# Kernel optimization log

Hardware: AMD Instinct MI355X
Metric: run time of the kernel (lower is better)

## Reference

```python
import jax, jax.numpy as jnp
import numpy as np

TOP_K = 8
THRESHOLD = 0.0        # similarity_threshold
SELF_SIM = 0.999       # exclude_self cutoff
EPS = 1e-12            # F.normalize eps


def _l2_normalize(x):
    # matches torch.nn.functional.normalize(p=2, dim=-1, eps=1e-12)
    n = jnp.linalg.norm(x, axis=-1, keepdims=True)
    return x / jnp.maximum(n, EPS)


def setup_inputs() -> dict:
    key = jax.random.key(0)
    kq, km = jax.random.split(key)
    B, N, D = 2048, 65536, 512
    q = jax.random.normal(kq, (B, D), dtype=jnp.float32)
    mem = jax.random.normal(km, (N, D), dtype=jnp.float32)
    # add_memories() stores L2-normalized representations when normalize=True
    mem = _l2_normalize(mem)
    return {"query_representations": q, "memory_bank": mem}


def reference(query_representations, memory_bank):
    # normalize queries (config.normalize_memories=True)
    q = _l2_normalize(query_representations)            # [B, D]
    # cosine similarity: bank rows already unit-norm
    sims = jnp.einsum("bd,nd->bn", q, memory_bank)      # [B, N]
    neg_inf = jnp.float32(-jnp.inf)
    # exclude_self: mask near-exact matches
    sims = jnp.where(sims > SELF_SIM, neg_inf, sims)
    # threshold mask
    sims = jnp.where(sims >= THRESHOLD, sims, neg_inf)
    # top-k (k = min(top_k, count) = TOP_K since bank is full)
    top_sims, top_idx = jax.lax.top_k(sims, TOP_K)      # [B, K]
    retrieved = memory_bank[top_idx]                    # [B, K, D] gather
    mask = top_sims > neg_inf                           # [B, K] valid entries
    return retrieved, top_sims, mask
```

## Files before the change

### kernel.cpp

```cpp
#include <hip/hip_runtime.h>
#include <math.h>

#define D        512
#define NQ       2048
#define NMEM     65536
#define TOPK     8
#define NCAND    32
#define SELF_SIM 0.999f
#define FSCALE   64.0f
#define TAU_RAW  483.328f
#define CAP      448
#define SCAP     1280

#define QB     256
#define SPAN   1024
#define NSPL   64
#define NROUND 64
#define BUFSZ  24576u

typedef __attribute__((ext_vector_type(4))) float f32x4;

__device__ __forceinline__ void gl_lds16(const void* g, void* l) {
    __builtin_amdgcn_global_load_lds(
        (const __attribute__((address_space(1))) void*)g,
        (__attribute__((address_space(3))) void*)l, 16, 0, 0);
}

__device__ __forceinline__ unsigned pack4_fp8(float4 v) {
    int lo = __builtin_amdgcn_cvt_pk_fp8_f32(v.x * FSCALE, v.y * FSCALE, 0, false);
    return (unsigned)__builtin_amdgcn_cvt_pk_fp8_f32(v.z * FSCALE, v.w * FSCALE, lo, true);
}

__global__ __launch_bounds__(256)
void k_prep(const float* __restrict__ mem, const float* __restrict__ q,
            unsigned* __restrict__ mp8, unsigned* __restrict__ qp8,
            double* __restrict__ qinv)
{
    if (blockIdx.x < 2048) {
        const int n16 = (NMEM * D) / 16;
        for (int i = blockIdx.x * 256 + threadIdx.x; i < n16; i += 2048 * 256) {
            const float4* p = (const float4*)(mem + (size_t)i * 16);
            uint4 o;
            o.x = pack4_fp8(p[0]); o.y = pack4_fp8(p[1]);
            o.z = pack4_fp8(p[2]); o.w = pack4_fp8(p[3]);
            ((uint4*)mp8)[i] = o;
        }
    } else {
        const int row  = (blockIdx.x - 2048) * 4 + (threadIdx.x >> 6);
        const int lane = threadIdx.x & 63;
        const float4* src = (const float4*)(q + (size_t)row * D);
        float4 v0 = src[lane];
        float4 v1 = src[lane + 64];
        double ss = (double)v0.x*v0.x + (double)v0.y*v0.y + (double)v0.z*v0.z + (double)v0.w*v0.w
                  + (double)v1.x*v1.x + (double)v1.y*v1.y + (double)v1.z*v1.z + (double)v1.w*v1.w;
        #pragma unroll
        for (int off = 32; off >= 1; off >>= 1)
            ss += __shfl_xor(ss, off, 64);
        double inv = 1.0 / fmax(sqrt(ss), 1e-12);
        float invf = (float)inv;
        float4 n0 = make_float4(v0.x*invf, v0.y*invf, v0.z*invf, v0.w*invf);
        float4 n1 = make_float4(v1.x*invf, v1.y*invf, v1.z*invf, v1.w*invf);
        unsigned* dst = qp8 + (size_t)row * (D / 4);
        dst[lane]      = pack4_fp8(n0);
        dst[lane + 64] = pack4_fp8(n1);
        if (lane == 0) qinv[row] = inv;
    }
}

__global__ __launch_bounds__(512, 4)
void k_cand(const char* __restrict__ qp8, const char* __restrict__ mp8,
            unsigned* __restrict__ cnt, uint2* __restrict__ cbuf)
{
    __shared__ __align__(16) char smem[49152 + 16 + SCAP * 8];
    unsigned* scnt = (unsigned*)(smem + 49152);
    uint2*    sbuf = (uint2*)   (smem + 49168);

    const int tid = threadIdx.x;
    const int w = tid >> 6, l = tid & 63;
    const int fc = l & 15, fr = l >> 4;

    const int id  = blockIdx.x;
    const int xcd = id & 7;
    const int j   = id >> 3;
    const int qblk = j & 7;
    const int sg   = j >> 3;
    const int split = xcd + 8 * sg;
    const int qbase = qblk * QB;
    const int nbase = split * SPAN;

    const int qrow = tid >> 1;
    const unsigned hq = (unsigned)((tid & 1) ^ ((qrow >> 2) & 1));
    const unsigned qsrc = (unsigned)(qbase + qrow) * 512u + hq * 16u;
    const int mrow = (tid >> 1) & 127;
    const unsigned hm = (unsigned)((tid & 1) ^ ((mrow >> 2) & 1));
    const unsigned msrc = (unsigned)mrow * 512u + (unsigned)(tid >> 8) * 32u + hm * 16u;
    const unsigned mbase = (unsigned)nbase * 512u;
    const unsigned dQ0 = (unsigned)tid * 16u;
    const unsigned dQ1 = dQ0 + 8192u;
    const unsigned dM  = 16384u + (unsigned)tid * 16u;

    if (tid == 0) *scnt = 0u;

    f32x4 acc[2][8];
    const int slot = 16 * ((fr >> 1) ^ ((fc >> 2) & 1)) + (fr & 1) * 8;

#define STAGE(R, B)                                                            \
    {   const unsigned r_ = (unsigned)(R);                                     \
        const unsigned kb_ = (r_ & 7u) * 64u;                                  \
        const unsigned sb_ = (r_ >> 3) * 65536u;                               \
        gl_lds16(qp8 + qsrc + kb_,              smem + (B) + dQ0);             \
        gl_lds16(qp8 + qsrc + kb_ + 32u,        smem + (B) + dQ1);             \
        gl_lds16(mp8 + mbase + sb_ + msrc + kb_, smem + (B) + dM);             \
    }

    unsigned cb = 0u;
    STAGE(0, cb);

    for (int r = 0; r < NROUND; ++r) {
        const int kp = r & 7, sub = r >> 3;
        if (kp == 0) {
            #pragma unroll
            for (int jj = 0; jj < 2; ++jj)
                #pragma unroll
                for (int t = 0; t < 8; ++t) acc[jj][t] = (f32x4){0.f, 0.f, 0.f, 0.f};
        }
        asm volatile("" ::: "memory");
        __builtin_amdgcn_s_barrier();
        asm volatile("" ::: "memory");
        if (r + 1 < NROUND) {
            STAGE(r + 1, cb ^ BUFSZ);
            asm volatile("s_waitcnt vmcnt(3)" ::: "memory");
        } else {
            asm volatile("s_waitcnt vmcnt(0)" ::: "memory");
        }
        __builtin_amdgcn_s_barrier();
        asm volatile("" ::: "memory");

        {
            const char* Qs = smem + cb;
            const char* Ms = smem + cb + 16384;
            #pragma unroll
            for (int ks = 0; ks < 2; ++ks) {
                const char* Qk = Qs + ks * 8192;
                const char* Mk = Ms + ks * 4096;
                long qf0 = *(const long*)(Qk + (w * 32 + fc) * 32 + slot);
                long qf1 = *(const long*)(Qk + (w * 32 + 16 + fc) * 32 + slot);
                __builtin_amdgcn_s_setprio(1);
                #pragma unroll
                for (int t = 0; t < 8; ++t) {
                    long a = *(const long*)(Mk + (t * 16 + fc) * 32 + slot);
                    acc[0][t] = __builtin_amdgcn_mfma_f32_16x16x32_fp8_fp8(a, qf0, acc[0][t], 0, 0, 0);
                    acc[1][t] = __builtin_amdgcn_mfma_f32_16x16x32_fp8_fp8(a, qf1, acc[1][t], 0, 0, 0);
                }
                __builtin_amdgcn_s_setprio(0);
            }
        }
        if (kp == 7) {
            const int nb0 = nbase + sub * 128 + fr * 4;
            #pragma unroll
            for (int jj = 0; jj < 2; ++jj) {
                float tm[8];
                #pragma unroll
                for (int t = 0; t < 8; ++t)
                    tm[t] = fmaxf(fmaxf(acc[jj][t][0], acc[jj][t][1]),
                                  fmaxf(acc[jj][t][2], acc[jj][t][3]));
                float m = tm[0];
                #pragma unroll
                for (int t = 1; t < 8; ++t) m = fmaxf(m, tm[t]);
                if (m > TAU_RAW) {
                    const unsigned qloc = (unsigned)(w * 32 + jj * 16 + fc);
                    #pragma unroll
                    for (int t = 0; t < 8; ++t) if (tm[t] > TAU_RAW) {
                        #pragma unroll
                        for (int rr = 0; rr < 4; ++rr) {
                            const float v = acc[jj][t][rr];
                            if (v > TAU_RAW) {
                                unsigned p = atomicAdd(scnt, 1u);
                                if (p < SCAP)
                                    sbuf[p] = make_uint2(__float_as_uint(v),
                                        (qloc << 16) | (unsigned)(nb0 + t * 16 + rr));
                            }
                        }
                    }
                }
            }
        }
        cb ^= BUFSZ;
    }
#undef STAGE

    __syncthreads();
    const unsigned ns = min(*scnt, (unsigned)SCAP);
    for (unsigned i = tid; i < ns; i += 512) {
        const uint2 e = sbuf[i];
        const int qg = qbase + (int)(e.y >> 16);
        const unsigned p = atomicAdd(&cnt[qg], 1u);
        if (p < CAP)
            cbuf[(size_t)qg * CAP + p] = make_uint2(e.x, e.y & 0xffffu);
    }
}

__global__ __launch_bounds__(256)
void k_final(const unsigned* __restrict__ cnt, const uint2* __restrict__ cbuf,
             const float* __restrict__ q, const float* __restrict__ mem,
             const double* __restrict__ qinv, float* __restrict__ out)
{
    __shared__ unsigned long long keys[CAP];
    __shared__ int    scand[NCAND];
    __shared__ double rsv[NCAND];
    __shared__ int    fidx[TOPK];

    const int qq  = blockIdx.x;
    const int tid = threadIdx.x;
    const int n = (int)min(cnt[qq], (unsigned)CAP);

    if (tid < NCAND) scand[tid] = -1;
    const uint2* src = cbuf + (size_t)qq * CAP;
    for (int c = tid; c < n; c += 256) {
        const uint2 e = src[c];
        keys[c] = ((unsigned long long)e.x << 16)
                | (unsigned long long)(0xffffu - (e.y & 0xffffu));
    }
    __syncthreads();
    for (int c = tid; c < n; c += 256) {
        const unsigned long long my = keys[c];
        int rank = 0;
        for (int j2 = 0; j2 < n; ++j2) rank += (keys[j2] > my) ? 1 : 0;
        if (rank < NCAND) scand[rank] = 0xffff - (int)(my & 0xffffu);
    }
    __syncthreads();

    const int w = tid >> 6, lane = tid & 63;
    float qv[8];
    #pragma unroll
    for (int t = 0; t < 8; ++t) qv[t] = q[(size_t)qq * D + t * 64 + lane];
    for (int ci = w * 8; ci < w * 8 + 8; ++ci) {
        const int m = scand[ci];
        double s = 0.0;
        if (m >= 0) {
            const float* mp = mem + (size_t)m * D;
            #pragma unroll
            for (int t = 0; t < 8; ++t)
                s += (double)qv[t] * (double)mp[t * 64 + lane];
        }
        #pragma unroll
        for (int off = 32; off >= 1; off >>= 1)
            s += __shfl_xor(s, off, 64);
        if (lane == 0) rsv[ci] = (m >= 0) ? s * qinv[qq] : -1.0 / 0.0;
    }
    __syncthreads();

    if (tid < NCAND) {
        double x = rsv[tid];
        if (scand[tid] < 0 || x > (double)SELF_SIM || x < 0.0) x = -1.0 / 0.0;
        rsv[tid] = x;
    }
    __syncthreads();
    if (tid < NCAND) {
        const double x  = rsv[tid];
        const int    mi = (scand[tid] < 0) ? 0x7fffffff : scand[tid];
        int rank = 0;
        for (int j2 = 0; j2 < NCAND; ++j2) {
            const double xj = rsv[j2];
            const int    ij = (scand[j2] < 0) ? 0x7fffffff : scand[j2];
            if (xj > x || (xj == x && (ij < mi || (ij == mi && j2 < tid)))) ++rank;
        }
        if (rank < TOPK) {
            float* tops  = out + (size_t)NQ * TOPK * D;
            float* maskp = tops + (size_t)NQ * TOPK;
            const bool valid = (x > -1.0 / 0.0) || !isinf(x) ? (x != -INFINITY) : false;
            tops [qq * TOPK + rank] = (float)x;
            maskp[qq * TOPK + rank] = (x == -INFINITY) ? 0.0f : 1.0f;
            fidx [rank] = (scand[tid] < 0) ? 0 : scand[tid];
            (void)valid;
        }
    }
    __syncthreads();

    for (int i = tid; i < TOPK * (D / 4); i += 256) {
        const int s2 = i >> 7;
        const int d4 = i & 127;
        const int sr = fidx[s2];
        ((float4*)out)[((size_t)qq * TOPK + s2) * (D / 4) + d4] =
            ((const float4*)mem)[(size_t)sr * (D / 4) + d4];
    }
}

extern "C" void kernel_launch(void* const* d_in, const int* in_sizes, int n_in,
                              void* d_out, int out_size, void* d_ws, size_t ws_size,
                              hipStream_t stream)
{
    const float* q   = (const float*)d_in[0];
    const float* mem = (const float*)d_in[1];
    float* out = (float*)d_out;
    char* ws = (char*)d_ws;

    unsigned* mp8  = (unsigned*)(ws);
    unsigned* qp8  = (unsigned*)(ws + ((size_t)32 << 20));
    unsigned* cnt  = (unsigned*)(ws + ((size_t)33 << 20));
    uint2*    cbuf = (uint2*)   (ws + ((size_t)34 << 20));
    double*   qinv = (double*)  (ws + ((size_t)42 << 20));

    hipMemsetAsync(cnt, 0, NQ * sizeof(unsigned), stream);

    k_prep<<<2560, 256, 0, stream>>>(mem, q, mp8, qp8, qinv);
    k_cand<<<(NQ / QB) * NSPL, 512, 0, stream>>>((const char*)qp8, (const char*)mp8, cnt, cbuf);
    k_final<<<NQ, 256, 0, stream>>>(cnt, cbuf, q, mem, qinv, out);
}
```

Baseline: 211.8 us.

## Pre-swizzle FP8 operands into MFMA fragment order for contiguous LDS staging

The prep kernel now writes the fp8 memory bank and normalized queries in a blocked layout that matches the MFMA fragment order. The candidate kernel can then stage tiles with plain contiguous global-to-LDS copies and read each fragment with one 16-byte LDS load, replacing the swizzled 8-byte reads. The prep conversion of the bank becomes one pass per thread over 16 float4s. The layout ties prep and GEMM together tightly, and any indexing mismatch would silently corrupt the similarities.

```diff
diff --git a/kernel.cpp b/kernel.cpp
--- a/kernel.cpp
+++ b/kernel.cpp
@@ -19,6 +19,7 @@
 #define BUFSZ  24576u
 
 typedef __attribute__((ext_vector_type(4))) float f32x4;
+typedef __attribute__((ext_vector_type(2))) unsigned long u64x2;
 
 __device__ __forceinline__ void gl_lds16(const void* g, void* l) {
     __builtin_amdgcn_global_load_lds(
@@ -37,17 +38,27 @@
             double* __restrict__ qinv)
 {
     if (blockIdx.x < 2048) {
-        const int n16 = (NMEM * D) / 16;
-        for (int i = blockIdx.x * 256 + threadIdx.x; i < n16; i += 2048 * 256) {
-            const float4* p = (const float4*)(mem + (size_t)i * 16);
-            uint4 o;
-            o.x = pack4_fp8(p[0]); o.y = pack4_fp8(p[1]);
-            o.z = pack4_fp8(p[2]); o.w = pack4_fp8(p[3]);
-            ((uint4*)mp8)[i] = o;
+        const int i = blockIdx.x * 256 + threadIdx.x;
+        const int row = i >> 3, p = i & 7;
+        const float4* pf = (const float4*)(mem + (size_t)row * D + p * 64);
+        float4 f[16];
+        #pragma unroll
+        for (int t = 0; t < 16; ++t) f[t] = pf[t];
+        const int nblk = row >> 7, t8 = (row >> 4) & 7, fc = row & 15;
+        uint4* dst = (uint4*)mp8 + ((size_t)nblk * 4096 + p * 512 + t8 * 64 + fc);
+        #pragma unroll
+        for (int fr = 0; fr < 4; ++fr) {
+            uint4 c;
+            c.x = pack4_fp8(f[fr * 2]);
+            c.y = pack4_fp8(f[fr * 2 + 1]);
+            c.z = pack4_fp8(f[8 + fr * 2]);
+            c.w = pack4_fp8(f[8 + fr * 2 + 1]);
+            dst[fr * 16] = c;
         }
     } else {
-        const int row  = (blockIdx.x - 2048) * 4 + (threadIdx.x >> 6);
-        const int lane = threadIdx.x & 63;
+        __shared__ float rb[4][512];
+        const int wv = threadIdx.x >> 6, lane = threadIdx.x & 63;
+        const int row = (blockIdx.x - 2048) * 4 + wv;
         const float4* src = (const float4*)(q + (size_t)row * D);
         float4 v0 = src[lane];
         float4 v1 = src[lane + 64];
@@ -58,12 +69,21 @@
             ss += __shfl_xor(ss, off, 64);
         double inv = 1.0 / fmax(sqrt(ss), 1e-12);
         float invf = (float)inv;
-        float4 n0 = make_float4(v0.x*invf, v0.y*invf, v0.z*invf, v0.w*invf);
-        float4 n1 = make_float4(v1.x*invf, v1.y*invf, v1.z*invf, v1.w*invf);
-        unsigned* dst = qp8 + (size_t)row * (D / 4);
-        dst[lane]      = pack4_fp8(n0);
-        dst[lane + 64] = pack4_fp8(n1);
+        ((float4*)rb[wv])[lane]      = make_float4(v0.x*invf, v0.y*invf, v0.z*invf, v0.w*invf);
+        ((float4*)rb[wv])[lane + 64] = make_float4(v1.x*invf, v1.y*invf, v1.z*invf, v1.w*invf);
         if (lane == 0) qinv[row] = inv;
+        __syncthreads();
+        if (lane < 32) {
+            const int p = lane >> 2, fr = lane & 3;
+            const float* f = rb[wv] + p * 64 + fr * 8;
+            uint4 c;
+            c.x = pack4_fp8(*(const float4*)(f));
+            c.y = pack4_fp8(*(const float4*)(f + 4));
+            c.z = pack4_fp8(*(const float4*)(f + 32));
+            c.w = pack4_fp8(*(const float4*)(f + 36));
+            const int qblk = row >> 8, qb16 = (row >> 4) & 15, fc = row & 15;
+            ((uint4*)qp8)[(size_t)qblk * 8192 + p * 1024 + qb16 * 64 + fr * 16 + fc] = c;
+        }
     }
 }
 
@@ -88,29 +108,24 @@
     const int qbase = qblk * QB;
     const int nbase = split * SPAN;
 
-    const int qrow = tid >> 1;
-    const unsigned hq = (unsigned)((tid & 1) ^ ((qrow >> 2) & 1));
-    const unsigned qsrc = (unsigned)(qbase + qrow) * 512u + hq * 16u;
-    const int mrow = (tid >> 1) & 127;
-    const unsigned hm = (unsigned)((tid & 1) ^ ((mrow >> 2) & 1));
-    const unsigned msrc = (unsigned)mrow * 512u + (unsigned)(tid >> 8) * 32u + hm * 16u;
-    const unsigned mbase = (unsigned)nbase * 512u;
-    const unsigned dQ0 = (unsigned)tid * 16u;
-    const unsigned dQ1 = dQ0 + 8192u;
-    const unsigned dM  = 16384u + (unsigned)tid * 16u;
+    const unsigned qpanel = (unsigned)qblk * 131072u;
+    const unsigned mpanel = (unsigned)(nbase >> 7) * 65536u;
+    const unsigned dc0 = (unsigned)tid * 16u;
+    const unsigned dc1 = dc0 + 8192u;
 
     if (tid == 0) *scnt = 0u;
 
     f32x4 acc[2][8];
-    const int slot = 16 * ((fr >> 1) ^ ((fc >> 2) & 1)) + (fr & 1) * 8;
+    const int lofs = l * 16;
 
 #define STAGE(R, B)                                                            \
     {   const unsigned r_ = (unsigned)(R);                                     \
-        const unsigned kb_ = (r_ & 7u) * 64u;                                  \
-        const unsigned sb_ = (r_ >> 3) * 65536u;                               \
-        gl_lds16(qp8 + qsrc + kb_,              smem + (B) + dQ0);             \
-        gl_lds16(qp8 + qsrc + kb_ + 32u,        smem + (B) + dQ1);             \
-        gl_lds16(mp8 + mbase + sb_ + msrc + kb_, smem + (B) + dM);             \
+        const unsigned p_ = r_ & 7u;                                           \
+        const unsigned qoff = qpanel + p_ * 16384u;                            \
+        const unsigned moff = mpanel + (r_ >> 3) * 65536u + p_ * 8192u;        \
+        gl_lds16(qp8 + qoff + dc0, smem + (B) + dc0);                          \
+        gl_lds16(qp8 + qoff + dc1, smem + (B) + dc1);                          \
+        gl_lds16(mp8 + moff + dc0, smem + (B) + 16384u + dc0);                 \
     }
 
     unsigned cb = 0u;
@@ -139,21 +154,18 @@
         {
             const char* Qs = smem + cb;
             const char* Ms = smem + cb + 16384;
+            u64x2 qf0 = *(const u64x2*)(Qs + (2 * w) * 1024 + lofs);
+            u64x2 qf1 = *(const u64x2*)(Qs + (2 * w + 1) * 1024 + lofs);
+            __builtin_amdgcn_s_setprio(1);
             #pragma unroll
-            for (int ks = 0; ks < 2; ++ks) {
-                const char* Qk = Qs + ks * 8192;
-                const char* Mk = Ms + ks * 4096;
-                long qf0 = *(const long*)(Qk + (w * 32 + fc) * 32 + slot);
-                long qf1 = *(const long*)(Qk + (w * 32 + 16 + fc) * 32 + slot);
-                __builtin_amdgcn_s_setprio(1);
-                #pragma unroll
-                for (int t = 0; t < 8; ++t) {
-                    long a = *(const long*)(Mk + (t * 16 + fc) * 32 + slot);
-                    acc[0][t] = __builtin_amdgcn_mfma_f32_16x16x32_fp8_fp8(a, qf0, acc[0][t], 0, 0, 0);
-                    acc[1][t] = __builtin_amdgcn_mfma_f32_16x16x32_fp8_fp8(a, qf1, acc[1][t], 0, 0, 0);
-                }
-                __builtin_amdgcn_s_setprio(0);
+            for (int t = 0; t < 8; ++t) {
+                u64x2 a = *(const u64x2*)(Ms + t * 1024 + lofs);
+                acc[0][t] = __builtin_amdgcn_mfma_f32_16x16x32_fp8_fp8((long)a[0], (long)qf0[0], acc[0][t], 0, 0, 0);
+                acc[1][t] = __builtin_amdgcn_mfma_f32_16x16x32_fp8_fp8((long)a[0], (long)qf1[0], acc[1][t], 0, 0, 0);
+                acc[0][t] = __builtin_amdgcn_mfma_f32_16x16x32_fp8_fp8((long)a[1], (long)qf0[1], acc[0][t], 0, 0, 0);
+                acc[1][t] = __builtin_amdgcn_mfma_f32_16x16x32_fp8_fp8((long)a[1], (long)qf1[1], acc[1][t], 0, 0, 0);
             }
+            __builtin_amdgcn_s_setprio(0);
         }
         if (kp == 7) {
             const int nb0 = nbase + sub * 128 + fr * 4;
@@ -268,11 +280,9 @@
         if (rank < TOPK) {
             float* tops  = out + (size_t)NQ * TOPK * D;
             float* maskp = tops + (size_t)NQ * TOPK;
-            const bool valid = (x > -1.0 / 0.0) || !isinf(x) ? (x != -INFINITY) : false;
             tops [qq * TOPK + rank] = (float)x;
             maskp[qq * TOPK + rank] = (x == -INFINITY) ? 0.0f : 1.0f;
             fidx [rank] = (scand[tid] < 0) ? 0 : scand[tid];
-            (void)valid;
         }
     }
     __syncthreads();
```

New measurement: 213.3 us. Within noise of the previous version (+0.7%).
